# Performance work log

Hardware: AMD Instinct MI355X
Metric: run time of the kernel (lower is better)

## Reference

```python
import jax, jax.numpy as jnp
import numpy as np

B, D, MAXC = 16384, 64, 8
NPROB, NCON, TDIM, HID = 50000, 2000, 1024, 256

def setup_inputs() -> dict:
    key = jax.random.key(0)
    ks = jax.random.split(key, 20)
    s = 0.02
    return {
        'prob_ids': jax.random.randint(ks[0], (B,), 0, NPROB),
        'related_concept_index': jax.random.randint(ks[1], (B, MAXC), 0, NCON),
        'filter0': jax.random.randint(ks[2], (B, MAXC), 0, 2),
        'h': jax.random.normal(ks[3], (B, D), jnp.float32),
        'emb': jax.random.normal(ks[4], (B, 2 * D), jnp.float32),
        'operate': jax.random.randint(ks[5], (B, 1), 0, 2).astype(jnp.float32),
        'exercise_text_emb': jax.random.normal(ks[6], (NPROB, TDIM), jnp.float32) * s,
        'concept_text_emb': jax.random.normal(ks[7], (NCON, TDIM), jnp.float32) * s,
        'W1': jax.random.normal(ks[8], (TDIM, HID), jnp.float32) * s,
        'b1': jnp.zeros((HID,), jnp.float32),
        'W2': jax.random.normal(ks[9], (HID, D), jnp.float32) * s,
        'b2': jnp.zeros((D,), jnp.float32),
        'Wp': jax.random.normal(ks[10], (5 * D, 1), jnp.float32) * s,
        'bp': jnp.zeros((1,), jnp.float32),
        'Wx': jax.random.normal(ks[11], (4 * D, 3 * D), jnp.float32) * s,
        'Wh': jax.random.normal(ks[12], (D, 3 * D), jnp.float32) * s,
        'bx': jnp.zeros((3 * D,), jnp.float32),
        'bh': jnp.zeros((3 * D,), jnp.float32),
    }

def reference(prob_ids, related_concept_index, filter0, h, emb, operate,
              exercise_text_emb, concept_text_emb,
              W1, b1, W2, b2, Wp, bp, Wx, Wh, bx, bh):
    def text_proj(x):  # 1024 -> 256 -> 64 (dropout off at inference)
        return jax.nn.relu(x @ W1 + b1) @ W2 + b2

    red_prob = text_proj(exercise_text_emb)      # [NPROB, D]
    red_con = text_proj(concept_text_emb)        # [NCON, D]

    related = red_con[related_concept_index]     # gather: [B, MAXC, D]

    # text weights: cosine similarity of raw BERT embs (torch eps=1e-8)
    q = exercise_text_emb[prob_ids]              # [B, 1024]
    c = concept_text_emb[related_concept_index]  # [B, MAXC, 1024]
    dot = jnp.einsum('bd,bmd->bm', q, c)
    qn = jnp.sqrt(jnp.sum(q * q, axis=-1))[:, None]
    cn = jnp.sqrt(jnp.sum(c * c, axis=-1))
    tw = dot / jnp.maximum(qn * cn, 1e-8)
    tw = jnp.where(filter0 == 0, jnp.float32(-1e9), tw)
    tw = jax.nn.softmax(tw, axis=1)              # [B, MAXC]

    rep = jnp.einsum('bmd,bm->bd', related, tw)  # weighted concept sum
    v = jnp.concatenate([red_prob[prob_ids], rep], axis=1)  # [B, 2D]

    # predictor: funcs(n_layer=1, dim*5, 1) ~ single Linear
    prob = jnp.concatenate([h, v, emb], axis=1) @ Wp + bp   # [B, 1]

    # update_state -> GRU cell (mygru: input 4D, hidden D)
    op = operate
    v_cat = jnp.concatenate([v * op, v * (1 - op)], axis=1)
    e_cat = jnp.concatenate([emb * (1 - op), emb * op], axis=1)
    x = v_cat + e_cat                             # [B, 4D]
    xg = x @ Wx + bx
    hg = h @ Wh + bh
    xr, xz, xn = jnp.split(xg, 3, axis=1)
    hr, hz, hn = jnp.split(hg, 3, axis=1)
    r = jax.nn.sigmoid(xr + hr)
    z = jax.nn.sigmoid(xz + hz)
    n = jnp.tanh(xn + r * hn)
    h_next = (1 - z) * n + z * h                  # [B, D]
    return (prob, h_next)
```

## Files before the change

### kernel.cpp

```cpp
#include <hip/hip_runtime.h>
#include <cstdint>
#include <cstddef>

typedef unsigned short u16;
typedef unsigned char u8;
typedef long long i64;
typedef unsigned long long u64;
typedef __bf16 bf16x8 __attribute__((ext_vector_type(8)));
typedef float f32x4 __attribute__((ext_vector_type(4)));
typedef float f32x2 __attribute__((ext_vector_type(2)));
typedef u16 u16x4 __attribute__((ext_vector_type(4)));
typedef u16 u16x8 __attribute__((ext_vector_type(8)));

#define B_ 16384
#define D_ 64
#define MAXC_ 8
#define NCON_ 2000
#define NCONP_ 2048
#define TDIM_ 1024
#define HID_ 256

#define VMW(n) asm volatile("s_waitcnt vmcnt(" #n ")" ::: "memory")
#define LGKM0 asm volatile("s_waitcnt lgkmcnt(0)" ::: "memory")
#define BAR() __builtin_amdgcn_s_barrier()

__device__ inline u16 f2b(float f){
  unsigned u = __float_as_uint(f);
  u += 0x7fffu + ((u >> 16) & 1u);
  return (u16)(u >> 16);
}
__device__ inline float b2f(u16 u){ return __uint_as_float(((unsigned)u) << 16); }

__device__ inline unsigned pk2fp8(float a, float b){
  return (unsigned)__builtin_amdgcn_cvt_pk_fp8_f32(a, b, 0, false);
}
template<bool HI>
__device__ inline f32x2 unpk_fp8(unsigned v){
  return __builtin_amdgcn_cvt_pk_f32_fp8(v, HI);
}

__device__ inline void gload16(const void* g, void* l){
  __builtin_amdgcn_global_load_lds((const __attribute__((address_space(1))) unsigned*)g,
                                   (__attribute__((address_space(3))) unsigned*)l, 16, 0, 0);
}

__device__ inline float wsum(float v){
  #pragma unroll
  for (int o = 32; o; o >>= 1) v += __shfl_xor(v, o);
  return v;
}
__device__ inline float sigf(float x){ return 1.f / (1.f + __expf(-x)); }

__global__ __launch_bounds__(256) void k_prep(
    const float* __restrict__ ex, const int* __restrict__ pid,
    const float* __restrict__ con,
    const float* __restrict__ W1, const float* __restrict__ W2,
    const float* __restrict__ Wx, const float* __restrict__ Wh,
    const float* __restrict__ bx, const float* __restrict__ bh,
    u8* __restrict__ qb8, float* __restrict__ qn,
    u8* __restrict__ cb8, float* __restrict__ cn,
    u16* __restrict__ W1T, u16* __restrict__ W2T, u16* __restrict__ WxhT,
    float* __restrict__ bxh)
{
  const int bid = blockIdx.x, tid = threadIdx.x;
  const int lane = tid & 63;
  if (bid < 4096){
    const int b = bid * 4 + (tid >> 6);
    const float* src = ex + (size_t)pid[b] * TDIM_;
    u8* dst8 = qb8 + (size_t)b * TDIM_;
    float ss = 0.f;
    #pragma unroll
    for (int c = 0; c < 4; ++c){
      float4 v = *(const float4*)(src + c * 256 + lane * 4);
      ss += v.x*v.x + v.y*v.y + v.z*v.z + v.w*v.w;
      unsigned lo = pk2fp8(v.x * 32.f, v.y * 32.f);
      unsigned hi = pk2fp8(v.z * 32.f, v.w * 32.f);
      *(unsigned*)(dst8 + c * 256 + lane * 4) = (lo & 0xffffu) | (hi << 16);
    }
    ss = wsum(ss);
    if (lane == 0) qn[b] = sqrtf(ss);
  } else if (bid < 4608){
    const int r = (bid - 4096) * 4 + (tid >> 6);
    u8* dst8 = cb8 + (size_t)r * TDIM_;
    if (r < NCON_){
      const float* src = con + (size_t)r * TDIM_;
      float ss = 0.f;
      #pragma unroll
      for (int c = 0; c < 4; ++c){
        float4 v = *(const float4*)(src + c * 256 + lane * 4);
        ss += v.x*v.x + v.y*v.y + v.z*v.z + v.w*v.w;
        unsigned lo = pk2fp8(v.x * 32.f, v.y * 32.f);
        unsigned hi = pk2fp8(v.z * 32.f, v.w * 32.f);
        *(unsigned*)(dst8 + c * 256 + lane * 4) = (lo & 0xffffu) | (hi << 16);
      }
      ss = wsum(ss);
      if (lane == 0) cn[r] = sqrtf(ss);
    } else {
      #pragma unroll
      for (int c = 0; c < 4; ++c)
        *(unsigned*)(dst8 + c * 256 + lane * 4) = 0u;
    }
  } else {
    int gid = (bid - 4608) * 256 + tid;
    if (gid < 262144){
      int n = gid >> 10, k = gid & 1023;
      W1T[gid] = f2b(W1[(size_t)k * 256 + n]);
    } else if (gid < 278528){
      int t = gid - 262144;
      int n = t >> 8, k = t & 255;
      W2T[t] = f2b(W2[(size_t)k * 64 + n]);
    } else if (gid < 360448){
      int t = gid - 278528;
      int c = t / 320, k = t % 320;
      int g = (c >> 4) & 3;
      int d = (c >> 6) * 16 + (c & 15);
      float v = 0.f;
      if (k < 256){
        if (g == 0)      v = Wx[(size_t)k * 192 + d];
        else if (g == 1) v = Wx[(size_t)k * 192 + 64 + d];
        else if (g == 2) v = Wx[(size_t)k * 192 + 128 + d];
      } else {
        int kh = k - 256;
        if (g == 0)      v = Wh[(size_t)kh * 192 + d];
        else if (g == 1) v = Wh[(size_t)kh * 192 + 64 + d];
        else if (g == 3) v = Wh[(size_t)kh * 192 + 128 + d];
      }
      WxhT[t] = f2b(v);
    } else if (gid < 360704){
      int c = gid - 360448;
      int g = (c >> 4) & 3;
      int d = (c >> 6) * 16 + (c & 15);
      float v;
      if (g == 0)      v = bx[d] + bh[d];
      else if (g == 1) v = bx[64 + d] + bh[64 + d];
      else if (g == 2) v = bx[128 + d];
      else             v = bh[128 + d];
      bxh[c] = v;
    }
  }
}

__global__ __launch_bounds__(512) void k_mlp(
    const u8* __restrict__ qb8, const u8* __restrict__ cb8,
    const u16* __restrict__ W1T, const float* __restrict__ b1,
    const u16* __restrict__ W2T, const float* __restrict__ b2,
    float* __restrict__ redq, float* __restrict__ redc)
{
  __shared__ u16 As[32 * 64];
  __shared__ u16 Bs[256 * 64];
  __shared__ u16 Hs[32 * 256];
  const int tid = threadIdx.x;
  const int lane = tid & 63;
  const int w = tid >> 6;
  const int lr = lane & 15, lq = lane >> 4;
  const bool qside = blockIdx.x < 512;
  const u8* Abase = qside ? qb8 : cb8;
  float* Obase = qside ? redq : redc;
  const int m0 = (qside ? (int)blockIdx.x : ((int)blockIdx.x - 512)) << 5;
  const int rf = w & 1, ch = w >> 1;
  const int arow = tid >> 3, asub = tid & 7;

  f32x4 acc[4] = {};
  for (int kt = 0; kt < 16; ++kt){
    if (tid < 256){
      u64 pk8 = *(const u64*)(Abase + (size_t)(m0 + arow) * 1024 + kt * 64 + (asub << 3));
      f32x2 p0 = unpk_fp8<false>((unsigned)pk8);
      f32x2 p1 = unpk_fp8<true >((unsigned)pk8);
      f32x2 p2 = unpk_fp8<false>((unsigned)(pk8 >> 32));
      f32x2 p3 = unpk_fp8<true >((unsigned)(pk8 >> 32));
      u16x8 o = { (u16)(__float_as_uint(p0[0]) >> 16), (u16)(__float_as_uint(p0[1]) >> 16),
                  (u16)(__float_as_uint(p1[0]) >> 16), (u16)(__float_as_uint(p1[1]) >> 16),
                  (u16)(__float_as_uint(p2[0]) >> 16), (u16)(__float_as_uint(p2[1]) >> 16),
                  (u16)(__float_as_uint(p3[0]) >> 16), (u16)(__float_as_uint(p3[1]) >> 16) };
      *(u16x8*)((char*)As + arow * 128 + ((asub << 4) ^ ((arow & 7) << 4))) = o;
    }
    #pragma unroll
    for (int i = 0; i < 4; ++i){
      int cc = i * 512 + tid;
      int r2 = cc >> 3, s2 = cc & 7;
      gload16(W1T + (size_t)r2 * 1024 + kt * 64 + ((s2 ^ (r2 & 7)) << 3), &Bs[cc * 8]);
    }
    VMW(0);
    LGKM0;
    BAR();
    #pragma unroll
    for (int ks = 0; ks < 2; ++ks){
      const int kb = ks * 64 + lq * 16;
      const int ra = rf * 16 + lr;
      bf16x8 af = *(const bf16x8*)((const char*)As + ra * 128 + (kb ^ ((ra & 7) << 4)));
      #pragma unroll
      for (int fc = 0; fc < 4; ++fc){
        int rb = ch * 64 + fc * 16 + lr;
        bf16x8 bf = *(const bf16x8*)((const char*)Bs + rb * 128 + (kb ^ ((rb & 7) << 4)));
        acc[fc] = __builtin_amdgcn_mfma_f32_16x16x32_bf16(af, bf, acc[fc], 0, 0, 0);
      }
    }
    BAR();
  }
  #pragma unroll
  for (int fc = 0; fc < 4; ++fc){
    int col = ch * 64 + fc * 16 + lr;
    float bv = b1[col];
    #pragma unroll
    for (int j = 0; j < 4; ++j){
      int rr = rf * 16 + lq * 4 + j;
      float v = fmaxf(acc[fc][j] * (1.f / 32.f) + bv, 0.f);
      *(u16*)((char*)Hs + rr * 512 + ((col * 2) ^ ((rr & 7) << 4))) = f2b(v);
    }
  }
  __syncthreads();
  const int rf2 = w & 1, cp = w >> 1;
  f32x4 acc2 = {};
  #pragma unroll
  for (int ks2 = 0; ks2 < 8; ++ks2){
    int rr = rf2 * 16 + lr;
    int kb2 = ks2 * 64 + lq * 16;
    bf16x8 af2 = *(const bf16x8*)((const char*)Hs + rr * 512 + (kb2 ^ ((rr & 7) << 4)));
    bf16x8 w2 = *(const bf16x8*)(W2T + (size_t)(cp * 16 + lr) * 256 + ks2 * 32 + lq * 8);
    acc2 = __builtin_amdgcn_mfma_f32_16x16x32_bf16(af2, w2, acc2, 0, 0, 0);
  }
  {
    int col = cp * 16 + lr;
    float bv = b2[col];
    #pragma unroll
    for (int j = 0; j < 4; ++j){
      int rr = m0 + rf2 * 16 + lq * 4 + j;
      Obase[(size_t)rr * 64 + col] = acc2[j] + bv;
    }
  }
}

__global__ __launch_bounds__(512) void k_mixgru(
    const u8* __restrict__ qb8, const u8* __restrict__ cb8,
    const float* __restrict__ qn, const float* __restrict__ cn,
    const int* __restrict__ rci, const int* __restrict__ filt,
    const float* __restrict__ redq, const float* __restrict__ redc,
    const float* __restrict__ h, const float* __restrict__ emb,
    const float* __restrict__ op, const float* __restrict__ Wp,
    const float* __restrict__ bp, const u16* __restrict__ WxhT,
    const float* __restrict__ bxh, float* __restrict__ prob_out,
    float* __restrict__ outh)
{
  __shared__ char SM[56320];
  u16*   XH   = (u16*)SM;
  float* DOTS = (float*)(SM + 20480);
  int*   SIDX = (int*)(SM + 21504);
  int*   SFLT = (int*)(SM + 22528);
  u8*    Cs   = (u8*)(SM + 23552);
  u8*    Qs8  = (u8*)(SM + 23552 + 16384);
  u16*   Bs   = (u16*)(SM + 23552);
  const int tid = threadIdx.x;
  const int lane = tid & 63;
  const int w = tid >> 6;
  const int m0 = blockIdx.x << 5;

  if (tid < 256) SIDX[tid] = rci[m0 * MAXC_ + tid];
  else           SFLT[tid - 256] = filt[m0 * MAXC_ + (tid - 256)];
  __syncthreads();

  const int R = w >> 2;
  const int cc0 = (w & 3) * 2;
  f32x4 dacc[2] = {};
  for (int kt = 0; kt < 16; ++kt){
    #pragma unroll
    for (int i = 0; i < 2; ++i){
      int e = i * 512 + tid;
      int slot = e >> 2, q4 = e & 3;
      int sw = (slot ^ (slot >> 2)) & 3;
      gload16(cb8 + (size_t)SIDX[slot] * TDIM_ + kt * 64 + ((q4 ^ sw) << 4),
              Cs + e * 16);
    }
    if (tid < 128){
      int slot = tid >> 2, q4 = tid & 3;
      int sw = (slot ^ (slot >> 2)) & 3;
      gload16(qb8 + (size_t)(m0 + slot) * TDIM_ + kt * 64 + ((q4 ^ sw) << 4),
              Qs8 + tid * 16);
    }
    VMW(0);
    BAR();
    #pragma unroll
    for (int ks = 0; ks < 2; ++ks){
      const int h8 = ks * 4 + (lane >> 4);
      const int arow = R * 16 + (lane & 15);
      const int asw = (arow ^ (arow >> 2)) & 3;
      i64 a = *(const i64*)(Qs8 + arow * 64 + (((h8 >> 1) ^ asw) << 4) + (h8 & 1) * 8);
      #pragma unroll
      for (int t = 0; t < 2; ++t){
        int slot = (R * 8 + cc0 + t) * 16 + (lane & 15);
        int bsw = (slot ^ (slot >> 2)) & 3;
        i64 bfr = *(const i64*)(Cs + slot * 64 + (((h8 >> 1) ^ bsw) << 4) + (h8 & 1) * 8);
        dacc[t] = __builtin_amdgcn_mfma_f32_16x16x32_fp8_fp8(a, bfr, dacc[t], 0, 0, 0);
      }
    }
    BAR();
  }
  #pragma unroll
  for (int t = 0; t < 2; ++t){
    const int cc = cc0 + t;
    const int col = lane & 15;
    #pragma unroll
    for (int j = 0; j < 4; ++j){
      int tr = (lane >> 4) * 4 + j;
      if (tr == 2 * cc && col < 8)       DOTS[(R * 16 + tr) * 8 + col] = dacc[t][j];
      if (tr == 2 * cc + 1 && col >= 8)  DOTS[(R * 16 + tr) * 8 + col - 8] = dacc[t][j];
    }
  }
  auto stageB = [&](int kt){
    #pragma unroll
    for (int i = 0; i < 4; ++i){
      int cc = i * 512 + tid;
      int r2 = cc >> 3, s2 = cc & 7;
      gload16(WxhT + (size_t)r2 * 320 + kt * 64 + ((s2 ^ (r2 & 7)) << 3), &Bs[cc * 8]);
    }
  };
  __syncthreads();
  stageB(0);

  for (int i = 0; i < 4; ++i){
    const int r = w * 4 + i;
    const int b = m0 + r;
    int idxm[MAXC_];
    #pragma unroll
    for (int m = 0; m < MAXC_; ++m) idxm[m] = SIDX[r * MAXC_ + m];
    const float qnb = qn[b];
    float sv[MAXC_]; float mx = -3.0e38f;
    #pragma unroll
    for (int m = 0; m < MAXC_; ++m){
      float dnm = fmaxf(qnb * cn[idxm[m]], 1e-8f);
      float s = (SFLT[r * MAXC_ + m] == 0) ? -1e9f
              : DOTS[r * 8 + m] * (1.f / 1024.f) / dnm;
      sv[m] = s; mx = fmaxf(mx, s);
    }
    float se = 0.f;
    #pragma unroll
    for (int m = 0; m < MAXC_; ++m){ sv[m] = __expf(sv[m] - mx); se += sv[m]; }
    const float inv = 1.f / se;
    float rep = 0.f;
    #pragma unroll
    for (int m = 0; m < MAXC_; ++m) rep += sv[m] * redc[(size_t)idxm[m] * D_ + lane];
    rep *= inv;
    const float v0 = redq[(size_t)b * D_ + lane];
    const float hv = h[(size_t)b * D_ + lane];
    const float e0 = emb[(size_t)b * 128 + lane];
    const float e1 = emb[(size_t)b * 128 + 64 + lane];
    float p = hv * Wp[lane] + v0 * Wp[64 + lane] + rep * Wp[128 + lane]
            + e0 * Wp[192 + lane] + e1 * Wp[256 + lane];
    p = wsum(p);
    if (lane == 0) prob_out[b] = p + bp[0];
    const float o = op[b], om = 1.f - o;
    auto xst = [&](int col, float v){
      *(u16*)((char*)XH + r * 640 + ((col * 2) ^ ((r & 7) << 4))) = f2b(v);
    };
    xst(lane,        v0 * o  + e0 * om);
    xst(64 + lane,   rep * o + e1 * om);
    xst(128 + lane,  v0 * om + e0 * o);
    xst(192 + lane,  rep * om + e1 * o);
    xst(256 + lane,  hv);
  }
  __syncthreads();

  const int lr = lane & 15, lq = lane >> 4;
  const int rh = w & 1, cc2 = w >> 1;
  f32x4 acc[4] = {};
  for (int kt = 0; kt < 5; ++kt){
    VMW(0);
    BAR();
    #pragma unroll
    for (int ks = 0; ks < 2; ++ks){
      const int kb = ks * 64 + lq * 16;
      int rra = rh * 16 + lr;
      bf16x8 af = *(const bf16x8*)((const char*)XH + rra * 640 +
                                   ((kt * 128 + kb) ^ ((rra & 7) << 4)));
      bf16x8 bfr[4];
      #pragma unroll
      for (int fc = 0; fc < 4; ++fc){
        int rr = cc2 * 64 + fc * 16 + lr;
        bfr[fc] = *(const bf16x8*)((const char*)Bs + rr * 128 + (kb ^ ((rr & 7) << 4)));
      }
      #pragma unroll
      for (int fc = 0; fc < 4; ++fc)
        acc[fc] = __builtin_amdgcn_mfma_f32_16x16x32_bf16(af, bfr[fc], acc[fc], 0, 0, 0);
    }
    BAR();
    if (kt < 4) stageB(kt + 1);
  }
  const int d = cc2 * 16 + lr;
  float bg[4];
  #pragma unroll
  for (int g = 0; g < 4; ++g) bg[g] = bxh[cc2 * 64 + g * 16 + lr];
  #pragma unroll
  for (int j = 0; j < 4; ++j){
    float rv = sigf(acc[0][j] + bg[0]);
    float zv = sigf(acc[1][j] + bg[1]);
    float nv = tanhf(acc[2][j] + bg[2] + rv * (acc[3][j] + bg[3]));
    int rr = m0 + rh * 16 + lq * 4 + j;
    float hv = h[(size_t)rr * 64 + d];
    outh[(size_t)rr * 64 + d] = (1.f - zv) * nv + zv * hv;
  }
}

extern "C" void kernel_launch(void* const* d_in, const int* in_sizes, int n_in,
                              void* d_out, int out_size, void* d_ws, size_t ws_size,
                              hipStream_t stream) {
  const int*   prob_ids = (const int*)  d_in[0];
  const int*   rci      = (const int*)  d_in[1];
  const int*   filt     = (const int*)  d_in[2];
  const float* h        = (const float*)d_in[3];
  const float* emb      = (const float*)d_in[4];
  const float* op       = (const float*)d_in[5];
  const float* ex       = (const float*)d_in[6];
  const float* con      = (const float*)d_in[7];
  const float* W1       = (const float*)d_in[8];
  const float* b1       = (const float*)d_in[9];
  const float* W2       = (const float*)d_in[10];
  const float* b2       = (const float*)d_in[11];
  const float* Wp       = (const float*)d_in[12];
  const float* bp       = (const float*)d_in[13];
  const float* Wx       = (const float*)d_in[14];
  const float* Wh       = (const float*)d_in[15];
  const float* bx       = (const float*)d_in[16];
  const float* bh       = (const float*)d_in[17];
  float* out = (float*)d_out;

  char* w = (char*)d_ws;
  size_t off = 0;
  auto alloc = [&](size_t bytes){ size_t o = off; off = (off + bytes + 255) & ~(size_t)255; return o; };
  u8*    qb8  = (u8*)   (w + alloc((size_t)B_ * TDIM_));
  u8*    cb8  = (u8*)   (w + alloc((size_t)NCONP_ * TDIM_));
  float* qn   = (float*)(w + alloc((size_t)B_ * 4));
  float* cn   = (float*)(w + alloc((size_t)NCONP_ * 4));
  float* redq = (float*)(w + alloc((size_t)B_ * D_ * 4));
  float* redc = (float*)(w + alloc((size_t)NCONP_ * D_ * 4));
  u16*   W1T  = (u16*)  (w + alloc((size_t)HID_ * TDIM_ * 2));
  u16*   W2T  = (u16*)  (w + alloc((size_t)D_ * HID_ * 2));
  u16*   WxhT = (u16*)  (w + alloc((size_t)256 * 320 * 2));
  float* bxh  = (float*)(w + alloc((size_t)256 * 4));

  k_prep<<<6017, 256, 0, stream>>>(ex, prob_ids, con, W1, W2, Wx, Wh, bx, bh,
                                   qb8, qn, cb8, cn, W1T, W2T, WxhT, bxh);
  k_mlp<<<576, 512, 0, stream>>>(qb8, cb8, W1T, b1, W2T, b2, redq, redc);
  k_mixgru<<<512, 512, 0, stream>>>(qb8, cb8, qn, cn, rci, filt, redq, redc,
                                    h, emb, op, Wp, bp, WxhT, bxh, out, out + B_);
}
```

Measured before the change: 80.24 us.

## Double-buffer concept gathers and preload full query rows in dot-product loop

The fp8 cosine-dot loop now double-buffers the gathered concept tiles, so the loads for the next k-tile are in flight while the MFMAs for the current tile run. The full 1024-byte query rows for the block's 32 rows are loaded into shared memory once up front with an XOR swizzle, instead of one slice per iteration. The goal is to hide gather latency behind compute. The cost is more shared memory (67.5KB instead of 55KB), which may lower occupancy. It also depends on the vmcnt(2) wait count matching the number of loads in flight, including the initial query loads.

```diff
diff --git a/kernel.cpp b/kernel.cpp
--- a/kernel.cpp
+++ b/kernel.cpp
@@ -241,49 +241,57 @@
     const float* __restrict__ bxh, float* __restrict__ prob_out,
     float* __restrict__ outh)
 {
-  __shared__ char SM[56320];
+  __shared__ char SM[67584];
+  u8*    QsF  = (u8*)SM;
   u16*   XH   = (u16*)SM;
   float* DOTS = (float*)(SM + 20480);
-  int*   SIDX = (int*)(SM + 21504);
-  int*   SFLT = (int*)(SM + 22528);
-  u8*    Cs   = (u8*)(SM + 23552);
-  u8*    Qs8  = (u8*)(SM + 23552 + 16384);
-  u16*   Bs   = (u16*)(SM + 23552);
+  int*   SIDX = (int*)(SM + 32768);
+  int*   SFLT = (int*)(SM + 33792);
+  u8*    CsB  = (u8*)(SM + 34816);
+  u16*   Bs   = (u16*)(SM + 34816);
   const int tid = threadIdx.x;
   const int lane = tid & 63;
   const int w = tid >> 6;
   const int m0 = blockIdx.x << 5;
 
+  #pragma unroll
+  for (int i = 0; i < 4; ++i){
+    int e = i * 512 + tid;
+    int row = e >> 6, c16 = e & 63;
+    gload16(qb8 + (size_t)(m0 + row) * TDIM_ + ((c16 ^ (row & 7)) << 4),
+            QsF + e * 16);
+  }
   if (tid < 256) SIDX[tid] = rci[m0 * MAXC_ + tid];
   else           SFLT[tid - 256] = filt[m0 * MAXC_ + (tid - 256)];
   __syncthreads();
 
-  const int R = w >> 2;
-  const int cc0 = (w & 3) * 2;
-  f32x4 dacc[2] = {};
-  for (int kt = 0; kt < 16; ++kt){
+  auto stageC = [&](int buf, int kt){
     #pragma unroll
     for (int i = 0; i < 2; ++i){
       int e = i * 512 + tid;
       int slot = e >> 2, q4 = e & 3;
       int sw = (slot ^ (slot >> 2)) & 3;
       gload16(cb8 + (size_t)SIDX[slot] * TDIM_ + kt * 64 + ((q4 ^ sw) << 4),
-              Cs + e * 16);
-    }
-    if (tid < 128){
-      int slot = tid >> 2, q4 = tid & 3;
-      int sw = (slot ^ (slot >> 2)) & 3;
-      gload16(qb8 + (size_t)(m0 + slot) * TDIM_ + kt * 64 + ((q4 ^ sw) << 4),
-              Qs8 + tid * 16);
-    }
-    VMW(0);
-    BAR();
+              CsB + buf * 16384 + e * 16);
+    }
+  };
+
+  const int R = w >> 2;
+  const int cc0 = (w & 3) * 2;
+  f32x4 dacc[2] = {};
+  stageC(0, 0);
+  int bufc = 0;
+  for (int kt = 0; kt < 16; ++kt){
+    if (kt < 15){ stageC(bufc ^ 1, kt + 1); VMW(2); }
+    else        { VMW(0); }
+    BAR();
+    const u8* Cs = CsB + bufc * 16384;
     #pragma unroll
     for (int ks = 0; ks < 2; ++ks){
       const int h8 = ks * 4 + (lane >> 4);
       const int arow = R * 16 + (lane & 15);
-      const int asw = (arow ^ (arow >> 2)) & 3;
-      i64 a = *(const i64*)(Qs8 + arow * 64 + (((h8 >> 1) ^ asw) << 4) + (h8 & 1) * 8);
+      const int c16r = kt * 4 + (h8 >> 1);
+      i64 a = *(const i64*)(QsF + arow * 1024 + ((c16r ^ (arow & 7)) << 4) + (h8 & 1) * 8);
       #pragma unroll
       for (int t = 0; t < 2; ++t){
         int slot = (R * 8 + cc0 + t) * 16 + (lane & 15);
@@ -293,6 +301,7 @@
       }
     }
     BAR();
+    bufc ^= 1;
   }
   #pragma unroll
   for (int t = 0; t < 2; ++t){
```

Result: faster. 78.13 us (-2.6%).
